# Optimization experiments

Measured on AMD Instinct MI355X. Metric: run time of the kernel, lower is better.

The kernel has to match this reference:

```python
import jax, jax.numpy as jnp
import numpy as np

B, C, H, W = 8, 128, 192, 192
CROP = 39
LEN = CROP // 2            # 19 -> 38x38 crop
CY = CX = 96               # fixed crop center (original draws random.randint(19, 173))
MARGIN = 1.0


def grid_sample_bilinear(img, grid):
    """Bilinear grid_sample, align_corners=True, zeros padding.
    img: (B,C,H,W); grid: (B,H,W,2) with (x,y) in [-1,1]."""
    _, _, Hi, Wi = img.shape
    gx = (grid[..., 0] + 1.0) * 0.5 * (Wi - 1)   # (B,H,W) source x
    gy = (grid[..., 1] + 1.0) * 0.5 * (Hi - 1)   # (B,H,W) source y
    x0 = jnp.floor(gx)
    y0 = jnp.floor(gy)

    def gather(xf, yf):
        valid = (xf >= 0) & (xf <= Wi - 1) & (yf >= 0) & (yf <= Hi - 1)
        xi = jnp.clip(xf, 0, Wi - 1).astype(jnp.int32)
        yi = jnp.clip(yf, 0, Hi - 1).astype(jnp.int32)
        # per-batch gather: (C,H,W) values at integer (y,x) locations
        v = jax.vmap(lambda im, y, x: im[:, y, x])(img, yi, xi)  # (B,C,H,W)
        return v * valid[:, None, :, :].astype(img.dtype)

    wx1 = gx - x0
    wx0 = 1.0 - wx1
    wy1 = gy - y0
    wy0 = 1.0 - wy1
    w = lambda a: a[:, None, :, :]
    return (w(wx0 * wy0) * gather(x0,       y0)
          + w(wx1 * wy0) * gather(x0 + 1.0, y0)
          + w(wx0 * wy1) * gather(x0,       y0 + 1.0)
          + w(wx1 * wy1) * gather(x0 + 1.0, y0 + 1.0))


def hardnet_loss(anchor, positive, margin=MARGIN):
    """loss_HardNet with anchor_swap=False, batch_reduce='min', triplet_margin."""
    d1 = jnp.sum(anchor * anchor, axis=1)                       # (N,)
    d2 = jnp.sum(positive * positive, axis=1)                   # (N,)
    sq = d1[:, None] + d2[None, :] - 2.0 * (anchor @ positive.T)  # (N,N)
    dm = jnp.sqrt(jnp.maximum(sq, 0.0) + 1e-6) + 1e-8
    n = dm.shape[0]
    pos = jnp.diagonal(dm)                                      # positive distances
    dmod = dm + jnp.eye(n, dtype=dm.dtype) * 10.0               # mask diagonal
    dmod = dmod + jnp.where(dmod < 0.008, 10.0, 0.0)            # mask near-duplicates
    min_neg = jnp.min(dmod, axis=1)                             # hardest negative per anchor
    return jnp.mean(jnp.maximum(margin + pos - min_neg, 0.0))


def setup_inputs() -> dict:
    key = jax.random.key(0)
    k1, k2, k3 = jax.random.split(key, 3)
    feat1 = jax.random.normal(k1, (B, C, H, W), dtype=jnp.float32)
    feat2 = jax.random.normal(k2, (B, C, H, W), dtype=jnp.float32)
    # absolute flow: pixel coordinates in [0, W-1] / [0, H-1]
    aflow = jax.random.uniform(k3, (B, 2, H, W), dtype=jnp.float32) * (W - 1)
    return {"feat1": feat1, "feat2": feat2, "aflow": aflow}


def reference(feat1, feat2, aflow):
    # _aflow_to_grid: pixel coords -> [-1,1] grid (align_corners=True convention)
    gx = aflow[:, 0] * (2.0 / (W - 1)) - 1.0
    gy = aflow[:, 1] * (2.0 / (H - 1)) - 1.0
    grid = jnp.stack([gx, gy], axis=-1)                          # (B,H,W,2)
    grid = jnp.where(jnp.isnan(grid), 9e9, grid)                 # invalid -> out of range
    feat2to1 = grid_sample_bilinear(feat2, grid)                 # warp img2 feats to img1
    s = slice(CY - LEN, CY + LEN)                                # fixed 38x38 crop
    f1 = feat1[:, :, s, s]
    f2 = feat2to1[:, :, s, s]
    a = f1.transpose(0, 2, 3, 1).reshape(-1, C)                  # (B*38*38, C)
    p = f2.transpose(0, 2, 3, 1).reshape(-1, C)
    return hardnet_loss(a, p)
```

## Files before the change

kernel.cpp:

```cpp
#include <hip/hip_runtime.h>
#include <stdint.h>

#define Hh 192
#define Ww 192
#define HW 36864
#define CROPW 38
#define CW2 1444
#define CROPOFF 77
#define NPTS 11552
#define NPAD 11776
#define NMT 92
#define NCT 92
#define NG 5
#define JPB 19
#define NBLK (NG*NMT)
#define SLABB 512
#define CROPB 304
#define BIGF 3.0e38f

typedef short bf16x8 __attribute__((ext_vector_type(8)));
typedef float f32x4 __attribute__((ext_vector_type(4)));
typedef uint32_t u32x4 __attribute__((ext_vector_type(4)));
typedef unsigned short ushort;

__device__ __forceinline__ ushort f2bf(float f) {
  uint32_t b = __float_as_uint(f);
  uint32_t r = b + 0x7fffu + ((b >> 16) & 1u);
  return (ushort)(r >> 16);
}
__device__ __forceinline__ float bf2f(ushort u) {
  return __uint_as_float(((uint32_t)u) << 16);
}

__device__ __forceinline__ void g2l16(const void* g, void* l) {
  __builtin_amdgcn_global_load_lds(
      (const __attribute__((address_space(1))) unsigned int*)g,
      (__attribute__((address_space(3))) unsigned int*)l, 16, 0, 0);
}

__global__ __launch_bounds__(1024) void fused_k(
    const float* __restrict__ feat1, const float* __restrict__ feat2,
    const float* __restrict__ aflow,
    ushort* __restrict__ aB, ushort* __restrict__ pB,
    float* __restrict__ d1, float* __restrict__ d2) {
  __shared__ __align__(16) uint32_t plane[HW];
  int bid = blockIdx.x;
  int t = threadIdx.x;

  if (bid < SLABB) {
    int b = bid >> 6, c = (bid & 63) * 2;
    const float* srcA = feat2 + ((size_t)(b*128 + c)) * HW;
    const float* srcB = srcA + HW;
    #pragma unroll
    for (int k = 0; k < 9; ++k) {
      int i = (k*1024 + t) * 4;
      f32x4 va = *(const f32x4*)(srcA + i);
      f32x4 vb = *(const f32x4*)(srcB + i);
      u32x4 pk;
      #pragma unroll
      for (int j = 0; j < 4; ++j)
        pk[j] = (uint32_t)f2bf(va[j]) | ((uint32_t)f2bf(vb[j]) << 16);
      *(u32x4*)&plane[i] = pk;
    }
    __syncthreads();
    int pbase = b*CW2;
    #pragma unroll
    for (int it = 0; it < 2; ++it) {
      int p = it*1024 + t;
      if (p < CW2) {
        int r = p / CROPW, cx = p % CROPW;
        int y = CROPOFF + r, x = CROPOFF + cx;
        float ax = aflow[((b*2 + 0)*Hh + y)*Ww + x];
        float ay = aflow[((b*2 + 1)*Hh + y)*Ww + x];
        float gxn = ax * (2.0f/(Ww-1)) - 1.0f;
        float gyn = ay * (2.0f/(Hh-1)) - 1.0f;
        float gx = (gxn + 1.0f) * 0.5f * (Ww-1);
        float gy = (gyn + 1.0f) * 0.5f * (Hh-1);
        int xi = min((int)floorf(gx), Ww-2);
        int yi = min((int)floorf(gy), Hh-2);
        float wx1 = gx - (float)xi, wx0 = 1.f - wx1;
        float wy1 = gy - (float)yi, wy0 = 1.f - wy1;
        int cell = yi*Ww + xi;
        uint32_t u00 = plane[cell];
        uint32_t u01 = plane[cell + 1];
        uint32_t u10 = plane[cell + Ww];
        uint32_t u11 = plane[cell + Ww + 1];
        float v0 = wy0*(wx0*bf2f((ushort)u00) + wx1*bf2f((ushort)u01))
                 + wy1*(wx0*bf2f((ushort)u10) + wx1*bf2f((ushort)u11));
        float v1 = wy0*(wx0*bf2f((ushort)(u00>>16)) + wx1*bf2f((ushort)(u01>>16)))
                 + wy1*(wx0*bf2f((ushort)(u10>>16)) + wx1*bf2f((ushort)(u11>>16)));
        ushort q0 = f2bf(v0), q1 = f2bf(v1);
        *(uint32_t*)&pB[(size_t)(pbase + p)*128 + c] = (uint32_t)q0 | ((uint32_t)q1 << 16);
        float f0 = bf2f(q0), f1 = bf2f(q1);
        atomicAdd(&d2[pbase + p], f0*f0 + f1*f1);
      }
    }
  } else if (bid < SLABB + CROPB) {
    ushort* lsh = (ushort*)plane;
    int rb2 = bid - SLABB;
    int b = rb2 / CROPW, r = rb2 % CROPW;
    int y = CROPOFF + r;
    {
      int xo = t & 63, cg = t >> 6;
      if (xo < CROPW) {
        const float* src = feat1 + ((size_t)b*128*HW) + (size_t)y*Ww + CROPOFF + xo;
        #pragma unroll
        for (int k = 0; k < 8; ++k) {
          int cc = cg + k*16;
          lsh[xo*136 + cc] = f2bf(src[(size_t)cc*HW]);
        }
      }
    }
    __syncthreads();
    int chunk = t & 7, p = t >> 3;
    if (p < CROPW) {
      int idx = b*CW2 + r*CROPW + p;
      ushort* dst = aB + (size_t)idx*128 + chunk*16;
      *(bf16x8*)dst       = *(const bf16x8*)&lsh[p*136 + chunk*16];
      *(bf16x8*)(dst + 8) = *(const bf16x8*)&lsh[p*136 + chunk*16 + 8];
      float s = 0.f;
      #pragma unroll
      for (int j = 0; j < 16; ++j) {
        float v = bf2f(lsh[p*136 + chunk*16 + j]);
        s += v*v;
      }
      s += __shfl_xor(s, 1); s += __shfl_xor(s, 2); s += __shfl_xor(s, 4);
      if (chunk == 0) d1[idx] = s;
    }
  } else {
    if (t < NPAD - NPTS) {
      int row = NPTS + t;
      u32x4 z = {0,0,0,0};
      #pragma unroll
      for (int c = 0; c < 8; ++c) {
        *(u32x4*)&aB[(size_t)row*128 + c*16] = z;
        *(u32x4*)&aB[(size_t)row*128 + c*16 + 8] = z;
        *(u32x4*)&pB[(size_t)row*128 + c*16] = z;
        *(u32x4*)&pB[(size_t)row*128 + c*16 + 8] = z;
      }
      d1[row] = 0.f;
      d2[row] = 1e30f;
    }
  }
}

__global__ __launch_bounds__(256) void gemmp_k(
    const ushort* __restrict__ aB, const ushort* __restrict__ pB,
    const float* __restrict__ d1, const float* __restrict__ d2,
    float* __restrict__ pos, float* __restrict__ pmin) {
  __shared__ __align__(16) ushort lB[2][128*128];

  int bid = blockIdx.x;
  int xcd = bid & 7, kk = bid >> 3;
  int start = (xcd < 4) ? xcd*58 : 232 + (xcd-4)*57;
  int L = start + kk;
  int g = L / NMT, tM = L % NMT;
  int j0 = g * JPB;
  int jn = (NCT - j0 < JPB) ? (NCT - j0) : JPB;

  int tid = threadIdx.x;
  int rowg = tid >> 4, cb = (tid & 15) << 4;
  int w = tid >> 6, l = tid & 63;
  int wr = w >> 1, wc = w & 1;
  int lcol = l & 15, hq = l >> 4, rb = hq << 2;
  int rsw = (lcol & 7) << 4;

  {
    const char* gB = (const char*)pB + (size_t)j0 * 128 * 256;
    #pragma unroll
    for (int rnd = 0; rnd < 8; ++rnd) {
      int row = rnd*16 + rowg;
      g2l16(gB + row*256 + (cb ^ ((row&7)<<4)), (char*)lB[0] + row*256 + cb);
    }
  }

  bf16x8 aF[16];
  {
    const char* gA = (const char*)aB + ((size_t)(tM*128 + wr*64 + lcol))*256 + hq*16;
    #pragma unroll
    for (int ma = 0; ma < 4; ++ma)
      #pragma unroll
      for (int ks = 0; ks < 4; ++ks)
        aF[ma*4+ks] = *(const bf16x8*)(gA + ma*16*256 + ks*64);
  }
  __syncthreads();

  float mPart[4] = {BIGF, BIGF, BIGF, BIGF};

  for (int it = 0; it < jn; ++it) {
    int j = j0 + it;
    if (it + 1 < jn) {
      const char* gB = (const char*)pB + (size_t)(j+1) * 128 * 256;
      char* dst = (char*)lB[(it+1) & 1];
      #pragma unroll
      for (int rnd = 0; rnd < 8; ++rnd) {
        int row = rnd*16 + rowg;
        g2l16(gB + row*256 + (cb ^ ((row&7)<<4)), dst + row*256 + cb);
      }
    }
    f32x4 d2v[4];
    #pragma unroll
    for (int np = 0; np < 4; ++np)
      d2v[np] = *(const f32x4*)&d2[j*128 + wc*64 + np*16 + rb];

    const char* bufB = (const char*)lB[it & 1];
    f32x4 acc[4][4] = {};
    #pragma unroll
    for (int ks = 0; ks < 4; ++ks) {
      int cbase = ks*64 + (hq << 4);
      bf16x8 bF[4];
      #pragma unroll
      for (int np = 0; np < 4; ++np)
        bF[np] = *(const bf16x8*)(bufB + (wc*64 + np*16 + lcol)*256 + (cbase ^ rsw));
      #pragma unroll
      for (int np = 0; np < 4; ++np)
        #pragma unroll
        for (int ma = 0; ma < 4; ++ma)
          acc[np][ma] = __builtin_amdgcn_mfma_f32_16x16x32_bf16(bF[np], aF[ma*4+ks], acc[np][ma], 0, 0, 0);
    }

    if (j != tM) {
      #pragma unroll
      for (int ma = 0; ma < 4; ++ma)
        #pragma unroll
        for (int np = 0; np < 4; ++np)
          #pragma unroll
          for (int reg = 0; reg < 4; ++reg)
            mPart[ma] = fminf(mPart[ma], fmaf(-2.f, acc[np][ma][reg], d2v[np][reg]));
    } else {
      #pragma unroll
      for (int ma = 0; ma < 4; ++ma) {
        int gi = tM*128 + wr*64 + ma*16 + lcol;
        #pragma unroll
        for (int np = 0; np < 4; ++np)
          #pragma unroll
          for (int reg = 0; reg < 4; ++reg) {
            int gj = j*128 + wc*64 + np*16 + rb + reg;
            float t = fmaf(-2.f, acc[np][ma][reg], d2v[np][reg]);
            if (gi == gj)
              pos[gi] = sqrtf(fmaxf(d1[gi] + t, 0.f) + 1e-6f) + 1e-8f;
            else
              mPart[ma] = fminf(mPart[ma], t);
          }
      }
    }
    __syncthreads();
  }

  #pragma unroll
  for (int ma = 0; ma < 4; ++ma) {
    float u = mPart[ma];
    u = fminf(u, __shfl_xor(u, 16));
    u = fminf(u, __shfl_xor(u, 32));
    mPart[ma] = u;
  }
  __syncthreads();
  float* sm = (float*)lB;
  if (hq == 0) {
    #pragma unroll
    for (int ma = 0; ma < 4; ++ma)
      sm[wc*128 + wr*64 + ma*16 + lcol] = mPart[ma];
  }
  __syncthreads();
  if (tid < 128) {
    int row = tM*128 + tid;
    float u = fminf(sm[tid], sm[128 + tid]);
    pmin[g*NPAD + row] = sqrtf(fmaxf(d1[row] + u, 0.f) + 1e-6f) + 1e-8f;
  }
}

__global__ __launch_bounds__(1024) void fin_k(const float* __restrict__ pos,
                                              const float* __restrict__ pmin,
                                              float* __restrict__ out) {
  float s = 0.f;
  for (int i = threadIdx.x; i < NPTS; i += 1024) {
    float p = pos[i];
    float mneg = p + 10.f;
    #pragma unroll
    for (int g = 0; g < NG; ++g) mneg = fminf(mneg, pmin[g*NPAD + i]);
    s += fmaxf(1.0f + p - mneg, 0.f);
  }
  for (int off = 1; off < 64; off <<= 1) s += __shfl_xor(s, off);
  __shared__ float red[16];
  if ((threadIdx.x & 63) == 0) red[threadIdx.x >> 6] = s;
  __syncthreads();
  if (threadIdx.x == 0) {
    float t = 0.f;
    #pragma unroll
    for (int k = 0; k < 16; ++k) t += red[k];
    out[0] = t / (float)NPTS;
  }
}

extern "C" void kernel_launch(void* const* d_in, const int* in_sizes, int n_in,
                              void* d_out, int out_size, void* d_ws, size_t ws_size,
                              hipStream_t stream) {
  const float* feat1 = (const float*)d_in[0];
  const float* feat2 = (const float*)d_in[1];
  const float* aflow = (const float*)d_in[2];

  char* ws = (char*)d_ws;
  ushort* aB = (ushort*)ws;
  ushort* pB = aB + (size_t)NPAD * 128;
  float*  d1 = (float*)(pB + (size_t)NPAD * 128);
  float*  d2 = d1 + NPAD;
  float*  pos = d2 + NPAD;
  float*  pmin = pos + NPAD;

  hipMemsetAsync(d2, 0, NPTS * sizeof(float), stream);
  hipLaunchKernelGGL(fused_k, dim3(SLABB + CROPB + 1), dim3(1024), 0, stream,
                     feat1, feat2, aflow, aB, pB, d1, d2);
  hipLaunchKernelGGL(gemmp_k, dim3(NBLK), dim3(256), 0, stream,
                     aB, pB, d1, d2, pos, pmin);
  hipLaunchKernelGGL(fin_k, dim3(1), dim3(1024), 0, stream,
                     pos, pmin, (float*)d_out);
}
```

Measured before the change: 89.96 us.

## Fuse final loss reduction into GEMM via last-block counter and pre-halve d2

Removes the separate single-block finalize kernel; instead each GEMM block increments a global counter after a threadfence and the last block performs the vectorised loss reduction. The d2 norms are stored halved so the epilogue uses a subtract instead of fmaf with -2, and the per-row min uses four independent min chains to shorten dependency latency. This saves one kernel launch and its gap, at the cost of atomics, fences and a serial tail in the last block.

```diff
diff --git a/kernel.cpp b/kernel.cpp
--- a/kernel.cpp
+++ b/kernel.cpp
@@ -42,7 +42,8 @@
     const float* __restrict__ feat1, const float* __restrict__ feat2,
     const float* __restrict__ aflow,
     ushort* __restrict__ aB, ushort* __restrict__ pB,
-    float* __restrict__ d1, float* __restrict__ d2) {
+    float* __restrict__ d1, float* __restrict__ d2,
+    unsigned* __restrict__ cnt) {
   __shared__ __align__(16) uint32_t plane[HW];
   int bid = blockIdx.x;
   int t = threadIdx.x;
@@ -92,7 +93,7 @@
         ushort q0 = f2bf(v0), q1 = f2bf(v1);
         *(uint32_t*)&pB[(size_t)(pbase + p)*128 + c] = (uint32_t)q0 | ((uint32_t)q1 << 16);
         float f0 = bf2f(q0), f1 = bf2f(q1);
-        atomicAdd(&d2[pbase + p], f0*f0 + f1*f1);
+        atomicAdd(&d2[pbase + p], 0.5f*(f0*f0 + f1*f1));
       }
     }
   } else if (bid < SLABB + CROPB) {
@@ -128,6 +129,7 @@
       if (chunk == 0) d1[idx] = s;
     }
   } else {
+    if (t == 0) *cnt = 0;
     if (t < NPAD - NPTS) {
       int row = NPTS + t;
       u32x4 z = {0,0,0,0};
@@ -139,16 +141,18 @@
         *(u32x4*)&pB[(size_t)row*128 + c*16 + 8] = z;
       }
       d1[row] = 0.f;
-      d2[row] = 1e30f;
+      d2[row] = 5e29f;
     }
   }
 }
 
 __global__ __launch_bounds__(256) void gemmp_k(
     const ushort* __restrict__ aB, const ushort* __restrict__ pB,
-    const float* __restrict__ d1, const float* __restrict__ d2,
-    float* __restrict__ pos, float* __restrict__ pmin) {
+    const float* __restrict__ d1, const float* __restrict__ hd2,
+    float* __restrict__ pos, float* __restrict__ pmin,
+    unsigned* __restrict__ cnt, float* __restrict__ out) {
   __shared__ __align__(16) ushort lB[2][128*128];
+  __shared__ int lastf;
 
   int bid = blockIdx.x;
   int xcd = bid & 7, kk = bid >> 3;
@@ -201,7 +205,7 @@
     f32x4 d2v[4];
     #pragma unroll
     for (int np = 0; np < 4; ++np)
-      d2v[np] = *(const f32x4*)&d2[j*128 + wc*64 + np*16 + rb];
+      d2v[np] = *(const f32x4*)&hd2[j*128 + wc*64 + np*16 + rb];
 
     const char* bufB = (const char*)lB[it & 1];
     f32x4 acc[4][4] = {};
@@ -221,12 +225,17 @@
 
     if (j != tM) {
       #pragma unroll
-      for (int ma = 0; ma < 4; ++ma)
-        #pragma unroll
-        for (int np = 0; np < 4; ++np)
-          #pragma unroll
-          for (int reg = 0; reg < 4; ++reg)
-            mPart[ma] = fminf(mPart[ma], fmaf(-2.f, acc[np][ma][reg], d2v[np][reg]));
+      for (int ma = 0; ma < 4; ++ma) {
+        float v0 = BIGF, v1 = BIGF, v2 = BIGF, v3 = BIGF;
+        #pragma unroll
+        for (int np = 0; np < 4; ++np) {
+          v0 = fminf(v0, d2v[np][0] - acc[np][ma][0]);
+          v1 = fminf(v1, d2v[np][1] - acc[np][ma][1]);
+          v2 = fminf(v2, d2v[np][2] - acc[np][ma][2]);
+          v3 = fminf(v3, d2v[np][3] - acc[np][ma][3]);
+        }
+        mPart[ma] = fminf(mPart[ma], fminf(fminf(v0, v1), fminf(v2, v3)));
+      }
     } else {
       #pragma unroll
       for (int ma = 0; ma < 4; ++ma) {
@@ -236,11 +245,12 @@
           #pragma unroll
           for (int reg = 0; reg < 4; ++reg) {
             int gj = j*128 + wc*64 + np*16 + rb + reg;
-            float t = fmaf(-2.f, acc[np][ma][reg], d2v[np][reg]);
-            if (gi == gj)
-              pos[gi] = sqrtf(fmaxf(d1[gi] + t, 0.f) + 1e-6f) + 1e-8f;
-            else
-              mPart[ma] = fminf(mPart[ma], t);
+            float q = d2v[np][reg] - acc[np][ma][reg];
+            if (gi == gj) {
+              pos[gi] = sqrtf(fmaxf(d1[gi] + 2.f*q, 0.f) + 1e-6f) + 1e-8f;
+              q = BIGF;
+            }
+            mPart[ma] = fminf(mPart[ma], q);
           }
       }
     }
@@ -265,30 +275,40 @@
   if (tid < 128) {
     int row = tM*128 + tid;
     float u = fminf(sm[tid], sm[128 + tid]);
-    pmin[g*NPAD + row] = sqrtf(fmaxf(d1[row] + u, 0.f) + 1e-6f) + 1e-8f;
-  }
-}
-
-__global__ __launch_bounds__(1024) void fin_k(const float* __restrict__ pos,
-                                              const float* __restrict__ pmin,
-                                              float* __restrict__ out) {
-  float s = 0.f;
-  for (int i = threadIdx.x; i < NPTS; i += 1024) {
-    float p = pos[i];
-    float mneg = p + 10.f;
-    #pragma unroll
-    for (int g = 0; g < NG; ++g) mneg = fminf(mneg, pmin[g*NPAD + i]);
-    s += fmaxf(1.0f + p - mneg, 0.f);
-  }
-  for (int off = 1; off < 64; off <<= 1) s += __shfl_xor(s, off);
-  __shared__ float red[16];
-  if ((threadIdx.x & 63) == 0) red[threadIdx.x >> 6] = s;
-  __syncthreads();
-  if (threadIdx.x == 0) {
-    float t = 0.f;
-    #pragma unroll
-    for (int k = 0; k < 16; ++k) t += red[k];
-    out[0] = t / (float)NPTS;
+    pmin[g*NPAD + row] = sqrtf(fmaxf(d1[row] + 2.f*u, 0.f) + 1e-6f) + 1e-8f;
+  }
+
+  __threadfence();
+  __syncthreads();
+  if (tid == 0) {
+    unsigned old = atomicAdd(cnt, 1u);
+    lastf = (old == NBLK - 1u);
+  }
+  __syncthreads();
+  if (lastf) {
+    __threadfence();
+    float s = 0.f;
+    for (int i = tid*4; i < NPTS; i += 1024) {
+      f32x4 p = *(const f32x4*)&pos[i];
+      f32x4 mn;
+      #pragma unroll
+      for (int jj = 0; jj < 4; ++jj) mn[jj] = p[jj] + 10.f;
+      #pragma unroll
+      for (int gg = 0; gg < NG; ++gg) {
+        f32x4 pm = *(const f32x4*)&pmin[gg*NPAD + i];
+        #pragma unroll
+        for (int jj = 0; jj < 4; ++jj) mn[jj] = fminf(mn[jj], pm[jj]);
+      }
+      #pragma unroll
+      for (int jj = 0; jj < 4; ++jj)
+        s += fmaxf(1.0f + p[jj] - mn[jj], 0.f);
+    }
+    for (int off = 1; off < 64; off <<= 1) s += __shfl_xor(s, off);
+    __syncthreads();
+    if (l == 0) sm[w] = s;
+    __syncthreads();
+    if (tid == 0)
+      out[0] = (sm[0] + sm[1] + sm[2] + sm[3]) / (float)NPTS;
   }
 }
 
@@ -306,12 +326,11 @@
   float*  d2 = d1 + NPAD;
   float*  pos = d2 + NPAD;
   float*  pmin = pos + NPAD;
+  unsigned* cnt = (unsigned*)(pmin + (size_t)NG*NPAD);
 
   hipMemsetAsync(d2, 0, NPTS * sizeof(float), stream);
   hipLaunchKernelGGL(fused_k, dim3(SLABB + CROPB + 1), dim3(1024), 0, stream,
-                     feat1, feat2, aflow, aB, pB, d1, d2);
+                     feat1, feat2, aflow, aB, pB, d1, d2, cnt);
   hipLaunchKernelGGL(gemmp_k, dim3(NBLK), dim3(256), 0, stream,
-                     aB, pB, d1, d2, pos, pmin);
-  hipLaunchKernelGGL(fin_k, dim3(1), dim3(1024), 0, stream,
-                     pos, pmin, (float*)d_out);
-}
+                     aB, pB, d1, d2, pos, pmin, cnt, (float*)d_out);
+}
```

After: 115.9 us. +28.8%, slower.

## Reshape gemmp warp tiling to 128x32 per wave and vectorize finalize

Applied to the files above, without the earlier changes.

Each of the four waves in the pairwise-distance GEMM now covers all 128 anchor rows and a 32-column slice of the positive tile, instead of a 2x2 split of 64x64. Each wave therefore reads fewer B fragments from LDS per MFMA but keeps twice as many A fragments in registers. The final cross-wave min reduction grows from two partials to four. Launch bounds now request two blocks per CU, which caps register use and risks spills with the larger aF array, and the finalize kernel reads its inputs as 4-wide vectors.

```diff
diff --git a/kernel.cpp b/kernel.cpp
--- a/kernel.cpp
+++ b/kernel.cpp
@@ -144,7 +144,7 @@
   }
 }
 
-__global__ __launch_bounds__(256) void gemmp_k(
+__global__ __launch_bounds__(256, 2) void gemmp_k(
     const ushort* __restrict__ aB, const ushort* __restrict__ pB,
     const float* __restrict__ d1, const float* __restrict__ d2,
     float* __restrict__ pos, float* __restrict__ pmin) {
@@ -161,7 +161,7 @@
   int tid = threadIdx.x;
   int rowg = tid >> 4, cb = (tid & 15) << 4;
   int w = tid >> 6, l = tid & 63;
-  int wr = w >> 1, wc = w & 1;
+  int wc = w;
   int lcol = l & 15, hq = l >> 4, rb = hq << 2;
   int rsw = (lcol & 7) << 4;
 
@@ -174,18 +174,18 @@
     }
   }
 
-  bf16x8 aF[16];
+  bf16x8 aF[32];
   {
-    const char* gA = (const char*)aB + ((size_t)(tM*128 + wr*64 + lcol))*256 + hq*16;
-    #pragma unroll
-    for (int ma = 0; ma < 4; ++ma)
+    const char* gA = (const char*)aB + ((size_t)(tM*128 + lcol))*256 + hq*16;
+    #pragma unroll
+    for (int ma = 0; ma < 8; ++ma)
       #pragma unroll
       for (int ks = 0; ks < 4; ++ks)
         aF[ma*4+ks] = *(const bf16x8*)(gA + ma*16*256 + ks*64);
   }
   __syncthreads();
 
-  float mPart[4] = {BIGF, BIGF, BIGF, BIGF};
+  float mPart[8] = {BIGF,BIGF,BIGF,BIGF,BIGF,BIGF,BIGF,BIGF};
 
   for (int it = 0; it < jn; ++it) {
     int j = j0 + it;
@@ -198,44 +198,44 @@
         g2l16(gB + row*256 + (cb ^ ((row&7)<<4)), dst + row*256 + cb);
       }
     }
-    f32x4 d2v[4];
-    #pragma unroll
-    for (int np = 0; np < 4; ++np)
-      d2v[np] = *(const f32x4*)&d2[j*128 + wc*64 + np*16 + rb];
+    f32x4 d2v[2];
+    #pragma unroll
+    for (int np = 0; np < 2; ++np)
+      d2v[np] = *(const f32x4*)&d2[j*128 + wc*32 + np*16 + rb];
 
     const char* bufB = (const char*)lB[it & 1];
-    f32x4 acc[4][4] = {};
+    f32x4 acc[2][8] = {};
     #pragma unroll
     for (int ks = 0; ks < 4; ++ks) {
       int cbase = ks*64 + (hq << 4);
-      bf16x8 bF[4];
-      #pragma unroll
-      for (int np = 0; np < 4; ++np)
-        bF[np] = *(const bf16x8*)(bufB + (wc*64 + np*16 + lcol)*256 + (cbase ^ rsw));
-      #pragma unroll
-      for (int np = 0; np < 4; ++np)
+      bf16x8 bF[2];
+      #pragma unroll
+      for (int np = 0; np < 2; ++np)
+        bF[np] = *(const bf16x8*)(bufB + (wc*32 + np*16 + lcol)*256 + (cbase ^ rsw));
+      #pragma unroll
+      for (int np = 0; np < 2; ++np)
         #pragma unroll
-        for (int ma = 0; ma < 4; ++ma)
+        for (int ma = 0; ma < 8; ++ma)
           acc[np][ma] = __builtin_amdgcn_mfma_f32_16x16x32_bf16(bF[np], aF[ma*4+ks], acc[np][ma], 0, 0, 0);
     }
 
     if (j != tM) {
       #pragma unroll
-      for (int ma = 0; ma < 4; ++ma)
+      for (int ma = 0; ma < 8; ++ma)
         #pragma unroll
-        for (int np = 0; np < 4; ++np)
+        for (int np = 0; np < 2; ++np)
           #pragma unroll
           for (int reg = 0; reg < 4; ++reg)
             mPart[ma] = fminf(mPart[ma], fmaf(-2.f, acc[np][ma][reg], d2v[np][reg]));
     } else {
       #pragma unroll
-      for (int ma = 0; ma < 4; ++ma) {
-        int gi = tM*128 + wr*64 + ma*16 + lcol;
+      for (int ma = 0; ma < 8; ++ma) {
+        int gi = tM*128 + ma*16 + lcol;
         #pragma unroll
-        for (int np = 0; np < 4; ++np)
+        for (int np = 0; np < 2; ++np)
           #pragma unroll
           for (int reg = 0; reg < 4; ++reg) {
-            int gj = j*128 + wc*64 + np*16 + rb + reg;
+            int gj = j*128 + wc*32 + np*16 + rb + reg;
             float t = fmaf(-2.f, acc[np][ma][reg], d2v[np][reg]);
             if (gi == gj)
               pos[gi] = sqrtf(fmaxf(d1[gi] + t, 0.f) + 1e-6f) + 1e-8f;
@@ -248,7 +248,7 @@
   }
 
   #pragma unroll
-  for (int ma = 0; ma < 4; ++ma) {
+  for (int ma = 0; ma < 8; ++ma) {
     float u = mPart[ma];
     u = fminf(u, __shfl_xor(u, 16));
     u = fminf(u, __shfl_xor(u, 32));
@@ -258,13 +258,14 @@
   float* sm = (float*)lB;
   if (hq == 0) {
     #pragma unroll
-    for (int ma = 0; ma < 4; ++ma)
-      sm[wc*128 + wr*64 + ma*16 + lcol] = mPart[ma];
+    for (int ma = 0; ma < 8; ++ma)
+      sm[wc*128 + ma*16 + lcol] = mPart[ma];
   }
   __syncthreads();
   if (tid < 128) {
     int row = tM*128 + tid;
-    float u = fminf(sm[tid], sm[128 + tid]);
+    float u = fminf(fminf(sm[tid], sm[128 + tid]),
+                    fminf(sm[256 + tid], sm[384 + tid]));
     pmin[g*NPAD + row] = sqrtf(fmaxf(d1[row] + u, 0.f) + 1e-6f) + 1e-8f;
   }
 }
@@ -273,12 +274,20 @@
                                               const float* __restrict__ pmin,
                                               float* __restrict__ out) {
   float s = 0.f;
-  for (int i = threadIdx.x; i < NPTS; i += 1024) {
-    float p = pos[i];
-    float mneg = p + 10.f;
-    #pragma unroll
-    for (int g = 0; g < NG; ++g) mneg = fminf(mneg, pmin[g*NPAD + i]);
-    s += fmaxf(1.0f + p - mneg, 0.f);
+  for (int i = threadIdx.x*4; i < NPTS; i += 4096) {
+    f32x4 p = *(const f32x4*)&pos[i];
+    f32x4 mn;
+    #pragma unroll
+    for (int jj = 0; jj < 4; ++jj) mn[jj] = p[jj] + 10.f;
+    #pragma unroll
+    for (int gg = 0; gg < NG; ++gg) {
+      f32x4 pm = *(const f32x4*)&pmin[gg*NPAD + i];
+      #pragma unroll
+      for (int jj = 0; jj < 4; ++jj) mn[jj] = fminf(mn[jj], pm[jj]);
+    }
+    #pragma unroll
+    for (int jj = 0; jj < 4; ++jj)
+      s += fmaxf(1.0f + p[jj] - mn[jj], 0.f);
   }
   for (int off = 1; off < 64; off <<= 1) s += __shfl_xor(s, off);
   __shared__ float red[16];
```

After: 88.79 us. Within noise of the previous version (-1.3%).
